# Performance work log

Measured on AMD Instinct MI355X. Metric: run time of the kernel, lower is better.

Reference implementation:

```python
import jax, jax.numpy as jnp
import numpy as np

B, T, C = 2, 2048, 2048
N_HEAD, N_GROUPS, HEAD_SIZE = 32, 8, 64
Q_PER_KV = N_HEAD // N_GROUPS
ROPE_N_ELEM = HEAD_SIZE  # rotary_percentage = 1.0
ROPE_BASE = 10000


def build_rope_cache(seq_len, n_elem, base=ROPE_BASE):
    theta = 1.0 / (base ** (jnp.arange(0, n_elem, 2, dtype=jnp.float32) / n_elem))
    idx_theta = jnp.outer(jnp.arange(seq_len, dtype=jnp.float32), theta)  # (T, n_elem/2)
    idx_theta = jnp.concatenate([idx_theta, idx_theta], axis=-1)  # (T, n_elem)
    return jnp.cos(idx_theta), jnp.sin(idx_theta)


def apply_rope(x, cos, sin):
    # x: (..., T, n_elem); cos/sin: (T, n_elem)
    h = x.shape[-1]
    x1, x2 = x[..., : h // 2], x[..., h // 2 :]
    rotated = jnp.concatenate([-x2, x1], axis=-1)
    return x * cos + rotated * sin


def setup_inputs() -> dict:
    key = jax.random.key(0)
    ks = jax.random.split(key, 5)
    x = jax.random.normal(ks[0], (B, T, C), dtype=jnp.float32)
    attn_w = jax.random.normal(ks[1], ((N_HEAD + 2 * N_GROUPS) * HEAD_SIZE, C), dtype=jnp.float32) * 0.02
    attn_b = jax.random.normal(ks[2], ((N_HEAD + 2 * N_GROUPS) * HEAD_SIZE,), dtype=jnp.float32) * 0.02
    proj_w = jax.random.normal(ks[3], (C, N_HEAD * HEAD_SIZE), dtype=jnp.float32) * 0.02
    proj_b = jax.random.normal(ks[4], (C,), dtype=jnp.float32) * 0.02
    cos, sin = build_rope_cache(T, ROPE_N_ELEM)
    return {"x": x, "cos": cos, "sin": sin, "attn_w": attn_w, "attn_b": attn_b,
            "proj_w": proj_w, "proj_b": proj_b}


def reference(x, cos, sin, attn_w, attn_b, proj_w, proj_b):
    b, t, _ = x.shape
    # fused QKV projection
    qkv = x @ attn_w.T + attn_b  # (B, T, (nh + 2g)*hs)
    qkv = qkv.reshape(b, t, N_GROUPS, Q_PER_KV + 2, HEAD_SIZE)
    qkv = qkv.transpose(0, 2, 3, 1, 4)  # (B, G, q_per_kv+2, T, hs)
    q = qkv[:, :, :Q_PER_KV]            # (B, G, q_per_kv, T, hs)
    k = qkv[:, :, Q_PER_KV]             # (B, G, T, hs)
    v = qkv[:, :, Q_PER_KV + 1]         # (B, G, T, hs)
    # RoPE (rope_n_elem == head_size, so applies to the full head dim)
    q = apply_rope(q, cos, sin)
    k = apply_rope(k, cos, sin)
    # grouped-query causal SDPA (equivalent to expanding k/v across q_per_kv)
    scale = 1.0 / jnp.sqrt(jnp.float32(HEAD_SIZE))
    scores = jnp.einsum("bgqtd,bgsd->bgqts", q, k) * scale  # (B,G,qk,T,T)
    causal = jnp.tril(jnp.ones((t, t), dtype=bool))
    scores = jnp.where(causal, scores, -jnp.inf)
    att = jax.nn.softmax(scores, axis=-1)
    y = jnp.einsum("bgqts,bgsd->bgqtd", att, v)  # (B,G,qk,T,hs)
    # merge (G, q_per_kv) -> n_head, then (B, T, nh*hs)
    y = y.reshape(b, N_HEAD, t, HEAD_SIZE).transpose(0, 2, 1, 3).reshape(b, t, N_HEAD * HEAD_SIZE)
    return y @ proj_w.T + proj_b


if __name__ == "__main__":
    out = reference(**setup_inputs())
    print(out.shape, out.dtype)
```

## Files before the change

### kernel.cpp

```cpp
#include <hip/hip_runtime.h>

#define T_SEQ 2048
#define CDIM  2048
#define NH    32
#define NG    8
#define HS    64
#define NQKV  3072
#define MROWS 4096
#define BATCH 2

typedef __bf16          bf16x8  __attribute__((ext_vector_type(8)));
typedef float           f32x4   __attribute__((ext_vector_type(4)));
typedef unsigned short  ushortx8 __attribute__((ext_vector_type(8)));
typedef unsigned short  ushortx4 __attribute__((ext_vector_type(4)));

__device__ __forceinline__ unsigned short f2bf(float f) {
    unsigned int u = __float_as_uint(f);
    u += 0x7fffu + ((u >> 16) & 1u);
    return (unsigned short)(u >> 16);
}
__device__ __forceinline__ float bf2f(unsigned short h) {
    return __uint_as_float(((unsigned int)h) << 16);
}
__device__ __forceinline__ bf16x8 as_bf(ushortx8 u) {
    return __builtin_bit_cast(bf16x8, u);
}
__device__ __forceinline__ void gload16(const void* g, void* l) {
    __builtin_amdgcn_global_load_lds(
        (const __attribute__((address_space(1))) unsigned int*)g,
        (__attribute__((address_space(3))) unsigned int*)l, 16, 0, 0);
}

__global__ void f2bf_vec(const float* __restrict__ in, unsigned short* __restrict__ out, int n4) {
    int i = blockIdx.x * blockDim.x + threadIdx.x;
    if (i < n4) {
        float4 v = ((const float4*)in)[i];
        ushortx4 o;
        o[0] = f2bf(v.x); o[1] = f2bf(v.y); o[2] = f2bf(v.z); o[3] = f2bf(v.w);
        ((ushortx4*)out)[i] = o;
    }
}

template<int MODE>
__global__ __launch_bounds__(256)
void gemm_bt(const unsigned short* __restrict__ A, const float* __restrict__ Bt,
             const float* __restrict__ bias, int M, int N, int K,
             float* __restrict__ Cout,
             unsigned short* __restrict__ Qb, unsigned short* __restrict__ Kb,
             unsigned short* __restrict__ Vb) {
    const int tid  = threadIdx.x;
    const int lane = tid & 63, w = tid >> 6;
    const int grp  = lane >> 4, cc = lane & 15;
    const int wm   = w >> 1, wn = w & 1;
    const int m0   = blockIdx.y * 128, n0 = blockIdx.x * 128;

    __shared__ unsigned short Al[128 * 48];
    __shared__ unsigned short Bl[128 * 48];

    f32x4 acc[4][4];
#pragma unroll
    for (int i = 0; i < 4; i++)
#pragma unroll
        for (int j = 0; j < 4; j++) acc[i][j] = (f32x4)0.0f;

    const int r0 = tid >> 2;
    const int k8 = (tid & 3) * 8;

    for (int k0 = 0; k0 < K; k0 += 32) {
        ushortx8 av0 = *(const ushortx8*)(A + (long)(m0 + r0)      * K + k0 + k8);
        ushortx8 av1 = *(const ushortx8*)(A + (long)(m0 + 64 + r0) * K + k0 + k8);
        const float* bp0 = Bt + (long)(n0 + r0)      * K + k0 + k8;
        const float* bp1 = Bt + (long)(n0 + 64 + r0) * K + k0 + k8;
        float4 b0a = *(const float4*)bp0, b0b = *(const float4*)(bp0 + 4);
        float4 b1a = *(const float4*)bp1, b1b = *(const float4*)(bp1 + 4);
        ushortx8 bv0, bv1;
        bv0[0] = f2bf(b0a.x); bv0[1] = f2bf(b0a.y); bv0[2] = f2bf(b0a.z); bv0[3] = f2bf(b0a.w);
        bv0[4] = f2bf(b0b.x); bv0[5] = f2bf(b0b.y); bv0[6] = f2bf(b0b.z); bv0[7] = f2bf(b0b.w);
        bv1[0] = f2bf(b1a.x); bv1[1] = f2bf(b1a.y); bv1[2] = f2bf(b1a.z); bv1[3] = f2bf(b1a.w);
        bv1[4] = f2bf(b1b.x); bv1[5] = f2bf(b1b.y); bv1[6] = f2bf(b1b.z); bv1[7] = f2bf(b1b.w);
        __syncthreads();
        *(ushortx8*)(Al + r0 * 48 + k8)        = av0;
        *(ushortx8*)(Al + (64 + r0) * 48 + k8) = av1;
        *(ushortx8*)(Bl + r0 * 48 + k8)        = bv0;
        *(ushortx8*)(Bl + (64 + r0) * 48 + k8) = bv1;
        __syncthreads();

        bf16x8 af[4], bfr[4];
#pragma unroll
        for (int mi = 0; mi < 4; mi++)
            af[mi] = as_bf(*(ushortx8*)(Al + (wm * 64 + mi * 16 + cc) * 48 + grp * 8));
#pragma unroll
        for (int ni = 0; ni < 4; ni++)
            bfr[ni] = as_bf(*(ushortx8*)(Bl + (wn * 64 + ni * 16 + cc) * 48 + grp * 8));
#pragma unroll
        for (int mi = 0; mi < 4; mi++)
#pragma unroll
            for (int ni = 0; ni < 4; ni++)
                acc[mi][ni] = __builtin_amdgcn_mfma_f32_16x16x32_bf16(af[mi], bfr[ni], acc[mi][ni], 0, 0, 0);
    }

    if (MODE == 1) {
#pragma unroll
        for (int ni = 0; ni < 4; ni++) {
            const int col = n0 + wn * 64 + ni * 16 + cc;
            const float bb = bias[col];
#pragma unroll
            for (int mi = 0; mi < 4; mi++) {
                const int row = m0 + wm * 64 + mi * 16 + grp * 4;
#pragma unroll
                for (int j = 0; j < 4; j++)
                    Cout[(long)(row + j) * N + col] = acc[mi][ni][j] + bb;
            }
        }
    } else {
        const int slot = (n0 + wn * 64) >> 6;
        const int g = slot / 6, s = slot % 6;
        const int b = m0 >> 11;
        const int t0 = (m0 & (T_SEQ - 1)) + wm * 64;
        unsigned short* dst;
        if (s < 4)        dst = Qb + (long)((b * NH + g * 4 + s) * T_SEQ) * HS;
        else if (s == 4)  dst = Kb + (long)((b * NG + g) * T_SEQ) * HS;
        else              dst = Vb + (long)((b * NG + g) * T_SEQ) * HS;
#pragma unroll
        for (int ni = 0; ni < 4; ni++) {
            const int d = ni * 16 + cc;
            const float bb = bias[slot * 64 + d];
#pragma unroll
            for (int mi = 0; mi < 4; mi++) {
                const int t = t0 + mi * 16 + grp * 4;
#pragma unroll
                for (int j = 0; j < 4; j++)
                    dst[(long)(t + j) * HS + d] = f2bf(acc[mi][ni][j] + bb);
            }
        }
    }
}

__global__ void rope_kernel(unsigned short* __restrict__ Qb, unsigned short* __restrict__ Kb,
                            const float* __restrict__ cosT, const float* __restrict__ sinT) {
    const float QSC = 0.125f * 1.44269504088896340736f;
    long idx = (long)blockIdx.x * blockDim.x + threadIdx.x;
    const long NQP = (long)BATCH * NH * T_SEQ * 32;
    const long NKP = (long)BATCH * NG * T_SEQ * 32;
    unsigned short* base; float sc; long r; int dp;
    if (idx < NQP)            { base = Qb; sc = QSC;  r = idx >> 5;          dp = (int)(idx & 31); }
    else if (idx < NQP + NKP) { long k = idx - NQP; base = Kb; sc = 1.0f; r = k >> 5; dp = (int)(k & 31); }
    else return;
    const int t = (int)(r & (T_SEQ - 1));
    unsigned short* p = base + r * 64;
    float x1 = bf2f(p[dp]), x2 = bf2f(p[dp + 32]);
    float cv = cosT[t * 64 + dp], sv = sinT[t * 64 + dp];
    p[dp]      = f2bf((x1 * cv - x2 * sv) * sc);
    p[dp + 32] = f2bf((x2 * cv + x1 * sv) * sc);
}

__global__ __launch_bounds__(256, 3)
void attn_kernel(const unsigned short* __restrict__ Qb, const unsigned short* __restrict__ Kb,
                 const unsigned short* __restrict__ Vb, unsigned short* __restrict__ Yb) {
    const int dsp = blockIdx.x;
    const int wk  = (dsp & 7) * 128 + (dsp >> 3);
    const int bx  = wk & 15;
    const int h   = (wk >> 4) & 31;
    const int b   = wk >> 9;

    const int tid = threadIdx.x, lane = tid & 63, w = tid >> 6;
    const int grp = lane >> 4, cc = lane & 15;
    const int g = h >> 2;
    const unsigned short* Qh = Qb + (long)((b * NH + h) * T_SEQ) * HS;
    const unsigned short* Kh = Kb + (long)((b * NG + g) * T_SEQ) * HS;
    const unsigned short* Vh = Vb + (long)((b * NG + g) * T_SEQ) * HS;
    const int q0  = bx * 128;
    const int qrb = q0 + w * 32;
    const int NT  = 2 * bx + 2;

    __shared__ unsigned short Kl[2][4096];
    __shared__ unsigned short Vt[2][64 * 72];
    __shared__ unsigned short Pl[4][32 * 72];

    bf16x8 aq[2][2];
#pragma unroll
    for (int qh = 0; qh < 2; qh++)
#pragma unroll
        for (int kh = 0; kh < 2; kh++)
            aq[qh][kh] = as_bf(*(const ushortx8*)(Qh + (long)(qrb + qh * 16 + cc) * HS + kh * 32 + grp * 8));

    const int U0 = (w * 2) * 64 + lane, U1 = U0 + 64;
    const int gk0 = (U0 >> 3) * 64 + (((U0 & 7) ^ ((U0 >> 3) & 7)) * 8);
    const int gk1 = (U1 >> 3) * 64 + (((U1 & 7) ^ ((U1 >> 3) & 7)) * 8);
    const int du0 = (w * 2) * 512, du1 = (w * 2 + 1) * 512;

    const int vp = tid & 31, vc = tid >> 5;
    const long vsrc = (long)(2 * vp) * HS + 8 * vc;

    f32x4 o[2][4];
#pragma unroll
    for (int qh = 0; qh < 2; qh++)
#pragma unroll
        for (int dt = 0; dt < 4; dt++) o[qh][dt] = (f32x4)0.0f;
    float mr[2][4], lr[2][4];
#pragma unroll
    for (int qh = 0; qh < 2; qh++)
#pragma unroll
        for (int j = 0; j < 4; j++) { mr[qh][j] = -1e30f; lr[qh][j] = 0.0f; }

    {
        gload16(Kh + gk0, &Kl[0][du0]);
        gload16(Kh + gk1, &Kl[0][du1]);
        ushortx8 v0 = *(const ushortx8*)(Vh + vsrc);
        ushortx8 v1 = *(const ushortx8*)(Vh + vsrc + HS);
#pragma unroll
        for (int e = 0; e < 8; e++) {
            unsigned int pk = (unsigned int)v0[e] | ((unsigned int)v1[e] << 16);
            *(unsigned int*)&Vt[0][(8 * vc + e) * 72 + 2 * vp] = pk;
        }
    }
    __syncthreads();

    for (int t = 0; t < NT; ++t) {
        const int cur = t & 1;
        const bool pre = (t + 1 < NT);
        ushortx8 v0, v1;
        if (pre) {
            const long kofs = (long)(t + 1) * 64 * HS;
            v0 = *(const ushortx8*)(Vh + kofs + vsrc);
            v1 = *(const ushortx8*)(Vh + kofs + vsrc + HS);
            gload16(Kh + kofs + gk0, &Kl[cur ^ 1][du0]);
            gload16(Kh + kofs + gk1, &Kl[cur ^ 1][du1]);
        }
        const int kv0 = t * 64;
        if (kv0 <= qrb + 31) {
            bf16x8 kf[4][2];
#pragma unroll
            for (int ct = 0; ct < 4; ct++)
#pragma unroll
                for (int kh = 0; kh < 2; kh++)
                    kf[ct][kh] = as_bf(*(const ushortx8*)&Kl[cur][(ct * 16 + cc) * 64 + (((kh * 4 + grp) ^ (cc & 7)) * 8)]);
            f32x4 s[2][4];
            __builtin_amdgcn_s_setprio(1);
#pragma unroll
            for (int qh = 0; qh < 2; qh++)
#pragma unroll
                for (int ct = 0; ct < 4; ct++) {
                    f32x4 a = (f32x4)0.0f;
                    a = __builtin_amdgcn_mfma_f32_16x16x32_bf16(aq[qh][0], kf[ct][0], a, 0, 0, 0);
                    a = __builtin_amdgcn_mfma_f32_16x16x32_bf16(aq[qh][1], kf[ct][1], a, 0, 0, 0);
                    s[qh][ct] = a;
                }
            __builtin_amdgcn_s_setprio(0);
            if (kv0 + 63 > qrb) {
#pragma unroll
                for (int qh = 0; qh < 2; qh++)
#pragma unroll
                    for (int ct = 0; ct < 4; ct++)
#pragma unroll
                        for (int j = 0; j < 4; j++) {
                            int col = kv0 + ct * 16 + cc, row = qrb + qh * 16 + grp * 4 + j;
                            if (col > row) s[qh][ct][j] = -1e30f;
                        }
            }
#pragma unroll
            for (int qh = 0; qh < 2; qh++) {
                float al[4];
#pragma unroll
                for (int j = 0; j < 4; j++) {
                    float v = fmaxf(fmaxf(s[qh][0][j], s[qh][1][j]), fmaxf(s[qh][2][j], s[qh][3][j]));
                    v = fmaxf(v, __shfl_xor(v, 1));
                    v = fmaxf(v, __shfl_xor(v, 2));
                    v = fmaxf(v, __shfl_xor(v, 4));
                    v = fmaxf(v, __shfl_xor(v, 8));
                    float mn = fmaxf(mr[qh][j], v);
                    al[j] = exp2f(mr[qh][j] - mn);
                    mr[qh][j] = mn;
                }
                float rs[4] = {0.f, 0.f, 0.f, 0.f};
#pragma unroll
                for (int ct = 0; ct < 4; ct++)
#pragma unroll
                    for (int j = 0; j < 4; j++) {
                        float p = exp2f(s[qh][ct][j] - mr[qh][j]);
                        s[qh][ct][j] = p; rs[j] += p;
                    }
#pragma unroll
                for (int j = 0; j < 4; j++) {
                    float v = rs[j];
                    v += __shfl_xor(v, 1); v += __shfl_xor(v, 2);
                    v += __shfl_xor(v, 4); v += __shfl_xor(v, 8);
                    lr[qh][j] = lr[qh][j] * al[j] + v;
                }
#pragma unroll
                for (int dt = 0; dt < 4; dt++)
#pragma unroll
                    for (int j = 0; j < 4; j++) o[qh][dt][j] *= al[j];
            }
#pragma unroll
            for (int qh = 0; qh < 2; qh++)
#pragma unroll
                for (int ct = 0; ct < 4; ct++)
#pragma unroll
                    for (int j = 0; j < 4; j++)
                        Pl[w][(qh * 16 + grp * 4 + j) * 72 + ct * 16 + cc] = f2bf(s[qh][ct][j]);
            bf16x8 pa[2][2];
#pragma unroll
            for (int qh = 0; qh < 2; qh++)
#pragma unroll
                for (int kc = 0; kc < 2; kc++)
                    pa[qh][kc] = as_bf(*(ushortx8*)&Pl[w][(qh * 16 + cc) * 72 + kc * 32 + grp * 8]);
            __builtin_amdgcn_s_setprio(1);
#pragma unroll
            for (int dt = 0; dt < 4; dt++) {
                bf16x8 vb[2];
#pragma unroll
                for (int kc = 0; kc < 2; kc++)
                    vb[kc] = as_bf(*(const ushortx8*)&Vt[cur][(dt * 16 + cc) * 72 + kc * 32 + grp * 8]);
#pragma unroll
                for (int qh = 0; qh < 2; qh++)
#pragma unroll
                    for (int kc = 0; kc < 2; kc++)
                        o[qh][dt] = __builtin_amdgcn_mfma_f32_16x16x32_bf16(pa[qh][kc], vb[kc], o[qh][dt], 0, 0, 0);
            }
            __builtin_amdgcn_s_setprio(0);
        }
        if (pre) {
#pragma unroll
            for (int e = 0; e < 8; e++) {
                unsigned int pk = (unsigned int)v0[e] | ((unsigned int)v1[e] << 16);
                *(unsigned int*)&Vt[cur ^ 1][(8 * vc + e) * 72 + 2 * vp] = pk;
            }
        }
        __syncthreads();
    }

#pragma unroll
    for (int qh = 0; qh < 2; qh++) {
        float inv[4];
#pragma unroll
        for (int j = 0; j < 4; j++) inv[j] = 1.0f / lr[qh][j];
#pragma unroll
        for (int dt = 0; dt < 4; dt++)
#pragma unroll
            for (int j = 0; j < 4; j++) {
                int row = qrb + qh * 16 + grp * 4 + j;
                Yb[((long)(b * T_SEQ + row)) * CDIM + h * HS + dt * 16 + cc] = f2bf(o[qh][dt][j] * inv[j]);
            }
    }
}

extern "C" void kernel_launch(void* const* d_in, const int* in_sizes, int n_in,
                              void* d_out, int out_size, void* d_ws, size_t ws_size,
                              hipStream_t stream) {
    const float* x      = (const float*)d_in[0];
    const float* cosT   = (const float*)d_in[1];
    const float* sinT   = (const float*)d_in[2];
    const float* attn_w = (const float*)d_in[3];
    const float* attn_b = (const float*)d_in[4];
    const float* proj_w = (const float*)d_in[5];
    const float* proj_b = (const float*)d_in[6];
    float* out = (float*)d_out;

    char* p = (char*)d_ws;
    unsigned short* XY = (unsigned short*)p; p += (size_t)MROWS * CDIM * 2;
    unsigned short* Qb = (unsigned short*)p; p += (size_t)BATCH * NH * T_SEQ * HS * 2;
    unsigned short* Kb = (unsigned short*)p; p += (size_t)BATCH * NG * T_SEQ * HS * 2;
    unsigned short* Vb = (unsigned short*)p; p += (size_t)BATCH * NG * T_SEQ * HS * 2;

    f2bf_vec<<<(MROWS * CDIM / 4 + 255) / 256, 256, 0, stream>>>(x, XY, MROWS * CDIM / 4);

    gemm_bt<0><<<dim3(NQKV / 128, MROWS / 128), 256, 0, stream>>>(
        XY, attn_w, attn_b, MROWS, NQKV, CDIM, nullptr, Qb, Kb, Vb);

    {
        long npairs = (long)BATCH * NH * T_SEQ * 32 + (long)BATCH * NG * T_SEQ * 32;
        rope_kernel<<<(int)((npairs + 255) / 256), 256, 0, stream>>>(Qb, Kb, cosT, sinT);
    }

    attn_kernel<<<dim3((T_SEQ / 128) * NH * BATCH), 256, 0, stream>>>(Qb, Kb, Vb, XY);

    gemm_bt<1><<<dim3(CDIM / 128, MROWS / 128), 256, 0, stream>>>(
        XY, proj_w, proj_b, MROWS, CDIM, CDIM, out, nullptr, nullptr, nullptr);
}
```

Before: 445.0 us.

## Pair causal q-tiles per block, fold row-sum into MFMA, lazy softmax rescale

```diff
diff --git a/kernel.cpp b/kernel.cpp
--- a/kernel.cpp
+++ b/kernel.cpp
@@ -158,10 +158,10 @@
 void attn_kernel(const unsigned short* __restrict__ Qb, const unsigned short* __restrict__ Kb,
                  const unsigned short* __restrict__ Vb, unsigned short* __restrict__ Yb) {
     const int dsp = blockIdx.x;
-    const int wk  = (dsp & 7) * 128 + (dsp >> 3);
-    const int bx  = wk & 15;
-    const int h   = (wk >> 4) & 31;
-    const int b   = wk >> 9;
+    const int wk  = (dsp & 7) * 64 + (dsp >> 3);
+    const int bxp = wk & 7;
+    const int h   = (wk >> 3) & 31;
+    const int b   = wk >> 8;
 
     const int tid = threadIdx.x, lane = tid & 63, w = tid >> 6;
     const int grp = lane >> 4, cc = lane & 15;
@@ -169,20 +169,16 @@
     const unsigned short* Qh = Qb + (long)((b * NH + h) * T_SEQ) * HS;
     const unsigned short* Kh = Kb + (long)((b * NG + g) * T_SEQ) * HS;
     const unsigned short* Vh = Vb + (long)((b * NG + g) * T_SEQ) * HS;
-    const int q0  = bx * 128;
-    const int qrb = q0 + w * 32;
-    const int NT  = 2 * bx + 2;
 
     __shared__ unsigned short Kl[2][4096];
-    __shared__ unsigned short Vt[2][64 * 72];
+    __shared__ unsigned short Vt[2][80 * 72];
     __shared__ unsigned short Pl[4][32 * 72];
 
-    bf16x8 aq[2][2];
-#pragma unroll
-    for (int qh = 0; qh < 2; qh++)
-#pragma unroll
-        for (int kh = 0; kh < 2; kh++)
-            aq[qh][kh] = as_bf(*(const ushortx8*)(Qh + (long)(qrb + qh * 16 + cc) * HS + kh * 32 + grp * 8));
+    for (int i = tid; i < 2 * 16 * 72; i += 256) {
+        int buf = i / (16 * 72), rem = i % (16 * 72);
+        int r = rem / 72, c = rem % 72;
+        Vt[buf][(64 + r) * 72 + c] = (r == 0) ? (unsigned short)0x3F80 : (unsigned short)0;
+    }
 
     const int U0 = (w * 2) * 64 + lane, U1 = U0 + 64;
     const int gk0 = (U0 >> 3) * 64 + (((U0 & 7) ^ ((U0 >> 3) & 7)) * 8);
@@ -192,156 +188,173 @@
     const int vp = tid & 31, vc = tid >> 5;
     const long vsrc = (long)(2 * vp) * HS + 8 * vc;
 
-    f32x4 o[2][4];
-#pragma unroll
-    for (int qh = 0; qh < 2; qh++)
-#pragma unroll
-        for (int dt = 0; dt < 4; dt++) o[qh][dt] = (f32x4)0.0f;
-    float mr[2][4], lr[2][4];
-#pragma unroll
-    for (int qh = 0; qh < 2; qh++)
-#pragma unroll
-        for (int j = 0; j < 4; j++) { mr[qh][j] = -1e30f; lr[qh][j] = 0.0f; }
-
-    {
-        gload16(Kh + gk0, &Kl[0][du0]);
-        gload16(Kh + gk1, &Kl[0][du1]);
-        ushortx8 v0 = *(const ushortx8*)(Vh + vsrc);
-        ushortx8 v1 = *(const ushortx8*)(Vh + vsrc + HS);
-#pragma unroll
-        for (int e = 0; e < 8; e++) {
-            unsigned int pk = (unsigned int)v0[e] | ((unsigned int)v1[e] << 16);
-            *(unsigned int*)&Vt[0][(8 * vc + e) * 72 + 2 * vp] = pk;
-        }
-    }
-    __syncthreads();
-
-    for (int t = 0; t < NT; ++t) {
-        const int cur = t & 1;
-        const bool pre = (t + 1 < NT);
-        ushortx8 v0, v1;
-        if (pre) {
-            const long kofs = (long)(t + 1) * 64 * HS;
-            v0 = *(const ushortx8*)(Vh + kofs + vsrc);
-            v1 = *(const ushortx8*)(Vh + kofs + vsrc + HS);
-            gload16(Kh + kofs + gk0, &Kl[cur ^ 1][du0]);
-            gload16(Kh + kofs + gk1, &Kl[cur ^ 1][du1]);
-        }
-        const int kv0 = t * 64;
-        if (kv0 <= qrb + 31) {
-            bf16x8 kf[4][2];
-#pragma unroll
-            for (int ct = 0; ct < 4; ct++)
-#pragma unroll
-                for (int kh = 0; kh < 2; kh++)
-                    kf[ct][kh] = as_bf(*(const ushortx8*)&Kl[cur][(ct * 16 + cc) * 64 + (((kh * 4 + grp) ^ (cc & 7)) * 8)]);
-            f32x4 s[2][4];
-            __builtin_amdgcn_s_setprio(1);
-#pragma unroll
-            for (int qh = 0; qh < 2; qh++)
-#pragma unroll
-                for (int ct = 0; ct < 4; ct++) {
-                    f32x4 a = (f32x4)0.0f;
-                    a = __builtin_amdgcn_mfma_f32_16x16x32_bf16(aq[qh][0], kf[ct][0], a, 0, 0, 0);
-                    a = __builtin_amdgcn_mfma_f32_16x16x32_bf16(aq[qh][1], kf[ct][1], a, 0, 0, 0);
-                    s[qh][ct] = a;
-                }
-            __builtin_amdgcn_s_setprio(0);
-            if (kv0 + 63 > qrb) {
-#pragma unroll
-                for (int qh = 0; qh < 2; qh++)
-#pragma unroll
-                    for (int ct = 0; ct < 4; ct++)
-#pragma unroll
-                        for (int j = 0; j < 4; j++) {
-                            int col = kv0 + ct * 16 + cc, row = qrb + qh * 16 + grp * 4 + j;
-                            if (col > row) s[qh][ct][j] = -1e30f;
-                        }
-            }
-#pragma unroll
-            for (int qh = 0; qh < 2; qh++) {
-                float al[4];
-#pragma unroll
-                for (int j = 0; j < 4; j++) {
-                    float v = fmaxf(fmaxf(s[qh][0][j], s[qh][1][j]), fmaxf(s[qh][2][j], s[qh][3][j]));
-                    v = fmaxf(v, __shfl_xor(v, 1));
-                    v = fmaxf(v, __shfl_xor(v, 2));
-                    v = fmaxf(v, __shfl_xor(v, 4));
-                    v = fmaxf(v, __shfl_xor(v, 8));
-                    float mn = fmaxf(mr[qh][j], v);
-                    al[j] = exp2f(mr[qh][j] - mn);
-                    mr[qh][j] = mn;
-                }
-                float rs[4] = {0.f, 0.f, 0.f, 0.f};
-#pragma unroll
-                for (int ct = 0; ct < 4; ct++)
-#pragma unroll
-                    for (int j = 0; j < 4; j++) {
-                        float p = exp2f(s[qh][ct][j] - mr[qh][j]);
-                        s[qh][ct][j] = p; rs[j] += p;
-                    }
-#pragma unroll
-                for (int j = 0; j < 4; j++) {
-                    float v = rs[j];
-                    v += __shfl_xor(v, 1); v += __shfl_xor(v, 2);
-                    v += __shfl_xor(v, 4); v += __shfl_xor(v, 8);
-                    lr[qh][j] = lr[qh][j] * al[j] + v;
-                }
-#pragma unroll
-                for (int dt = 0; dt < 4; dt++)
-#pragma unroll
-                    for (int j = 0; j < 4; j++) o[qh][dt][j] *= al[j];
-            }
-#pragma unroll
-            for (int qh = 0; qh < 2; qh++)
-#pragma unroll
-                for (int ct = 0; ct < 4; ct++)
-#pragma unroll
-                    for (int j = 0; j < 4; j++)
-                        Pl[w][(qh * 16 + grp * 4 + j) * 72 + ct * 16 + cc] = f2bf(s[qh][ct][j]);
-            bf16x8 pa[2][2];
-#pragma unroll
-            for (int qh = 0; qh < 2; qh++)
-#pragma unroll
-                for (int kc = 0; kc < 2; kc++)
-                    pa[qh][kc] = as_bf(*(ushortx8*)&Pl[w][(qh * 16 + cc) * 72 + kc * 32 + grp * 8]);
-            __builtin_amdgcn_s_setprio(1);
-#pragma unroll
-            for (int dt = 0; dt < 4; dt++) {
-                bf16x8 vb[2];
-#pragma unroll
-                for (int kc = 0; kc < 2; kc++)
-                    vb[kc] = as_bf(*(const ushortx8*)&Vt[cur][(dt * 16 + cc) * 72 + kc * 32 + grp * 8]);
-#pragma unroll
-                for (int qh = 0; qh < 2; qh++)
-#pragma unroll
-                    for (int kc = 0; kc < 2; kc++)
-                        o[qh][dt] = __builtin_amdgcn_mfma_f32_16x16x32_bf16(pa[qh][kc], vb[kc], o[qh][dt], 0, 0, 0);
-            }
-            __builtin_amdgcn_s_setprio(0);
-        }
-        if (pre) {
+    for (int pass = 0; pass < 2; ++pass) {
+        const int qtile = pass ? (15 - bxp) : bxp;
+        const int q0  = qtile * 128;
+        const int qrb = q0 + w * 32;
+        const int NT  = 2 * qtile + 2;
+
+        bf16x8 aq[2][2];
+#pragma unroll
+        for (int qh = 0; qh < 2; qh++)
+#pragma unroll
+            for (int kh = 0; kh < 2; kh++)
+                aq[qh][kh] = as_bf(*(const ushortx8*)(Qh + (long)(qrb + qh * 16 + cc) * HS + kh * 32 + grp * 8));
+
+        f32x4 o[2][5];
+#pragma unroll
+        for (int qh = 0; qh < 2; qh++)
+#pragma unroll
+            for (int dt = 0; dt < 5; dt++) o[qh][dt] = (f32x4)0.0f;
+        float mr[2][4];
+#pragma unroll
+        for (int qh = 0; qh < 2; qh++)
+#pragma unroll
+            for (int j = 0; j < 4; j++) mr[qh][j] = -1e30f;
+
+        {
+            gload16(Kh + gk0, &Kl[0][du0]);
+            gload16(Kh + gk1, &Kl[0][du1]);
+            ushortx8 v0 = *(const ushortx8*)(Vh + vsrc);
+            ushortx8 v1 = *(const ushortx8*)(Vh + vsrc + HS);
 #pragma unroll
             for (int e = 0; e < 8; e++) {
                 unsigned int pk = (unsigned int)v0[e] | ((unsigned int)v1[e] << 16);
-                *(unsigned int*)&Vt[cur ^ 1][(8 * vc + e) * 72 + 2 * vp] = pk;
+                *(unsigned int*)&Vt[0][(8 * vc + e) * 72 + 2 * vp] = pk;
             }
         }
         __syncthreads();
-    }
-
-#pragma unroll
-    for (int qh = 0; qh < 2; qh++) {
-        float inv[4];
-#pragma unroll
-        for (int j = 0; j < 4; j++) inv[j] = 1.0f / lr[qh][j];
-#pragma unroll
-        for (int dt = 0; dt < 4; dt++)
+
+        for (int t = 0; t < NT; ++t) {
+            const int cur = t & 1;
+            const bool pre = (t + 1 < NT);
+            ushortx8 v0, v1;
+            if (pre) {
+                const long kofs = (long)(t + 1) * 64 * HS;
+                v0 = *(const ushortx8*)(Vh + kofs + vsrc);
+                v1 = *(const ushortx8*)(Vh + kofs + vsrc + HS);
+                gload16(Kh + kofs + gk0, &Kl[cur ^ 1][du0]);
+                gload16(Kh + kofs + gk1, &Kl[cur ^ 1][du1]);
+            }
+            const int kv0 = t * 64;
+            if (kv0 <= qrb + 31) {
+                bf16x8 kf[4][2];
+#pragma unroll
+                for (int ct = 0; ct < 4; ct++)
+#pragma unroll
+                    for (int kh = 0; kh < 2; kh++)
+                        kf[ct][kh] = as_bf(*(const ushortx8*)&Kl[cur][(ct * 16 + cc) * 64 + (((kh * 4 + grp) ^ (cc & 7)) * 8)]);
+                f32x4 s[2][4];
+                __builtin_amdgcn_s_setprio(1);
+#pragma unroll
+                for (int qh = 0; qh < 2; qh++)
+#pragma unroll
+                    for (int ct = 0; ct < 4; ct++) {
+                        f32x4 a = (f32x4)0.0f;
+                        a = __builtin_amdgcn_mfma_f32_16x16x32_bf16(aq[qh][0], kf[ct][0], a, 0, 0, 0);
+                        a = __builtin_amdgcn_mfma_f32_16x16x32_bf16(aq[qh][1], kf[ct][1], a, 0, 0, 0);
+                        s[qh][ct] = a;
+                    }
+                __builtin_amdgcn_s_setprio(0);
+                if (kv0 + 63 > qrb) {
+#pragma unroll
+                    for (int qh = 0; qh < 2; qh++)
+#pragma unroll
+                        for (int ct = 0; ct < 4; ct++)
+#pragma unroll
+                            for (int j = 0; j < 4; j++) {
+                                int col = kv0 + ct * 16 + cc, row = qrb + qh * 16 + grp * 4 + j;
+                                if (col > row) s[qh][ct][j] = -1e30f;
+                            }
+                }
+#pragma unroll
+                for (int qh = 0; qh < 2; qh++) {
+                    float pm[4];
+#pragma unroll
+                    for (int j = 0; j < 4; j++) {
+                        float v = fmaxf(fmaxf(s[qh][0][j], s[qh][1][j]), fmaxf(s[qh][2][j], s[qh][3][j]));
+                        v = fmaxf(v, __shfl_xor(v, 1));
+                        v = fmaxf(v, __shfl_xor(v, 2));
+                        v = fmaxf(v, __shfl_xor(v, 4));
+                        v = fmaxf(v, __shfl_xor(v, 8));
+                        pm[j] = v;
+                    }
+                    bool need = false;
+#pragma unroll
+                    for (int j = 0; j < 4; j++) need |= (pm[j] > mr[qh][j] + 8.0f);
+                    if (__any(need)) {
+                        float al[4];
+#pragma unroll
+                        for (int j = 0; j < 4; j++) {
+                            float mn = fmaxf(mr[qh][j], pm[j]);
+                            al[j] = exp2f(mr[qh][j] - mn);
+                            mr[qh][j] = mn;
+                        }
+#pragma unroll
+                        for (int dt = 0; dt < 5; dt++)
+#pragma unroll
+                            for (int j = 0; j < 4; j++) o[qh][dt][j] *= al[j];
+                    }
+#pragma unroll
+                    for (int ct = 0; ct < 4; ct++)
+#pragma unroll
+                        for (int j = 0; j < 4; j++)
+                            s[qh][ct][j] = exp2f(s[qh][ct][j] - mr[qh][j]);
+                }
+#pragma unroll
+                for (int qh = 0; qh < 2; qh++)
+#pragma unroll
+                    for (int ct = 0; ct < 4; ct++)
+#pragma unroll
+                        for (int j = 0; j < 4; j++)
+                            Pl[w][(qh * 16 + grp * 4 + j) * 72 + ct * 16 + cc] = f2bf(s[qh][ct][j]);
+                bf16x8 pa[2][2];
+#pragma unroll
+                for (int qh = 0; qh < 2; qh++)
+#pragma unroll
+                    for (int kc = 0; kc < 2; kc++)
+                        pa[qh][kc] = as_bf(*(ushortx8*)&Pl[w][(qh * 16 + cc) * 72 + kc * 32 + grp * 8]);
+                __builtin_amdgcn_s_setprio(1);
+#pragma unroll
+                for (int dt = 0; dt < 5; dt++) {
+                    bf16x8 vb[2];
+#pragma unroll
+                    for (int kc = 0; kc < 2; kc++)
+                        vb[kc] = as_bf(*(const ushortx8*)&Vt[cur][(dt * 16 + cc) * 72 + kc * 32 + grp * 8]);
+#pragma unroll
+                    for (int qh = 0; qh < 2; qh++)
+#pragma unroll
+                        for (int kc = 0; kc < 2; kc++)
+                            o[qh][dt] = __builtin_amdgcn_mfma_f32_16x16x32_bf16(pa[qh][kc], vb[kc], o[qh][dt], 0, 0, 0);
+                }
+                __builtin_amdgcn_s_setprio(0);
+            }
+            if (pre) {
+#pragma unroll
+                for (int e = 0; e < 8; e++) {
+                    unsigned int pk = (unsigned int)v0[e] | ((unsigned int)v1[e] << 16);
+                    *(unsigned int*)&Vt[cur ^ 1][(8 * vc + e) * 72 + 2 * vp] = pk;
+                }
+            }
+            __syncthreads();
+        }
+
+#pragma unroll
+        for (int qh = 0; qh < 2; qh++) {
+            float inv[4];
 #pragma unroll
             for (int j = 0; j < 4; j++) {
-                int row = qrb + qh * 16 + grp * 4 + j;
-                Yb[((long)(b * T_SEQ + row)) * CDIM + h * HS + dt * 16 + cc] = f2bf(o[qh][dt][j] * inv[j]);
-            }
+                float lrv = __shfl(o[qh][4][j], (lane & 48));
+                inv[j] = 1.0f / lrv;
+            }
+#pragma unroll
+            for (int dt = 0; dt < 4; dt++)
+#pragma unroll
+                for (int j = 0; j < 4; j++) {
+                    int row = qrb + qh * 16 + grp * 4 + j;
+                    Yb[((long)(b * T_SEQ + row)) * CDIM + h * HS + dt * 16 + cc] = f2bf(o[qh][dt][j] * inv[j]);
+                }
+        }
     }
 }
 
@@ -373,7 +386,7 @@
         rope_kernel<<<(int)((npairs + 255) / 256), 256, 0, stream>>>(Qb, Kb, cosT, sinT);
     }
 
-    attn_kernel<<<dim3((T_SEQ / 128) * NH * BATCH), 256, 0, stream>>>(Qb, Kb, Vb, XY);
+    attn_kernel<<<dim3((T_SEQ / 128 / 2) * NH * BATCH), 256, 0, stream>>>(Qb, Kb, Vb, XY);
 
     gemm_bt<1><<<dim3(CDIM / 128, MROWS / 128), 256, 0, stream>>>(
         XY, proj_w, proj_b, MROWS, CDIM, CDIM, out, nullptr, nullptr, nullptr);
```

Measured after the change: 399.7 us. 1.11x faster.
